# Kernel tuning notes

Measured on AMD Instinct MI355X. Metric: run time of the kernel, lower is better.

## Reference

```python
import jax, jax.numpy as jnp
import numpy as np

TEMPERATURE = 1.0  # init kwarg
B, D = 8192, 128


def setup_inputs() -> dict:
    key = jax.random.key(0)
    k1, k2 = jax.random.split(key)
    sk = jax.random.normal(k1, (B, D), dtype=jnp.float32)
    im = jax.random.normal(k2, (B, D), dtype=jnp.float32)
    return {"sk": sk, "im": im}


def reference(sk, im):
    # The torch module builds a [2B,2B] Euclidean distance matrix over the
    # interleaved [sk_0, im_0, sk_1, im_1, ...] rows, then via the eye-mask /
    # repeat_interleave / [:,1::2] / good_indices / [::2] gather chain selects,
    # for each anchor i, logits row = [-d(sk_i, im_i)/T] ++ [-d(sk_i, im_j)/T, j != i]
    # with label 0, followed by mean cross-entropy.  Since cross-entropy only
    # depends on {row values} and which entry is positive, this is exactly:
    #   loss = mean_i( logsumexp_j(-d(sk_i, im_j)/T) - (-d(sk_i, im_i)/T) )
    # so we only need the [B,B] sk-vs-im distance block (dist_type == 0).
    sq = (
        jnp.sum(sk * sk, axis=1)[:, None]
        + jnp.sum(im * im, axis=1)[None, :]
        - 2.0 * (sk @ im.T)
    )  # [B, B] squared distances
    d = jnp.sqrt(jnp.maximum(sq, 0.0))
    logits = -d / TEMPERATURE  # [B, B]
    lse = jax.nn.logsumexp(logits, axis=1)  # [B]
    loss = jnp.mean(lse - jnp.diagonal(logits))
    return loss
```

## Files before the change

kernel.cpp:

```cpp
#include <hip/hip_runtime.h>
#include <math.h>

#define NB 8192
#define ND 128
#define GSTEP 64
#define NSTEP 4
#define NJB 32

#define C2F 2.0813689810056077f
#define NC2 (-4.1627379620112154f)

typedef float f32x4 __attribute__((ext_vector_type(4)));

typedef __attribute__((address_space(3))) void lds_void_t;
typedef __attribute__((address_space(1))) const void gconst_void_t;

__device__ __forceinline__ unsigned f2bf(float f) {
    union { float f; unsigned u; } v; v.f = f;
    unsigned r = v.u + 0x7FFFu + ((v.u >> 16) & 1u);
    return r >> 16;
}

__global__ void __launch_bounds__(256) prep_kernel(
    const float* __restrict__ sk, const float* __restrict__ im,
    unsigned* __restrict__ skb8, unsigned* __restrict__ imb8,
    float* __restrict__ skn, float* __restrict__ imn,
    float* __restrict__ diag, float* __restrict__ gacc,
    unsigned* __restrict__ ticket) {
    if (blockIdx.x == 0 && threadIdx.x == 0) { *gacc = 0.f; *ticket = 0u; }
    const int wave = threadIdx.x >> 6, lane = threadIdx.x & 63;
    const int half = lane >> 5, l32 = lane & 31;
    const int row = blockIdx.x * 8 + wave * 2 + half;
    const size_t off = (size_t)row * 128 + l32 * 4;
    const float4 a = *reinterpret_cast<const float4*>(sk + off);
    const float4 b = *reinterpret_cast<const float4*>(im + off);
    unsigned pa = 0, pb = 0;
    pa = __builtin_amdgcn_cvt_pk_fp8_f32(a.x, a.y, pa, false);
    pa = __builtin_amdgcn_cvt_pk_fp8_f32(a.z, a.w, pa, true);
    pb = __builtin_amdgcn_cvt_pk_fp8_f32(b.x, b.y, pb, false);
    pb = __builtin_amdgcn_cvt_pk_fp8_f32(b.z, b.w, pb, true);
    skb8[row * 32 + l32] = pa;
    imb8[row * 32 + l32] = pb;
    float sa = a.x * a.x + a.y * a.y + a.z * a.z + a.w * a.w;
    float sb = b.x * b.x + b.y * b.y + b.z * b.z + b.w * b.w;
    float dx = a.x - b.x, dy = a.y - b.y, dz = a.z - b.z, dw = a.w - b.w;
    float sd = dx * dx + dy * dy + dz * dz + dw * dw;
#pragma unroll
    for (int st = 1; st < 32; st <<= 1) {
        sa += __shfl_xor(sa, st);
        sb += __shfl_xor(sb, st);
        sd += __shfl_xor(sd, st);
    }
    if (l32 == 0) {
        skn[row] = sa * C2F;
        imn[row] = sb * C2F;
        diag[row] = sqrtf(sd);
    }
}

__global__ void __launch_bounds__(256, 5) tile_kernel(
    const unsigned char* __restrict__ skb8, const unsigned char* __restrict__ imb8,
    const float* __restrict__ skn, const float* __restrict__ imn,
    float* __restrict__ partial) {
    __shared__ unsigned char Ast[2][GSTEP * ND];

    const int t = threadIdx.x;
    const int w = t >> 6, lane = t & 63;
    const int hi = lane >> 4, lo = lane & 15;
    const int iw = blockIdx.x * 128 + w * 32;
    const int jg0 = blockIdx.y * (GSTEP * NSTEP);

    long bfr[2][4];
#pragma unroll
    for (int n = 0; n < 2; ++n) {
        const unsigned char* bp = skb8 + (size_t)(iw + n * 16 + lo) * ND + hi * 8;
#pragma unroll
        for (int kk = 0; kk < 4; ++kk)
            bfr[n][kk] = *reinterpret_cast<const long*>(bp + kk * 32);
    }
    float skv[2];
#pragma unroll
    for (int n = 0; n < 2; ++n) skv[n] = skn[iw + n * 16 + lo];

#define STAGE_A(buf, jrow0)                                                       \
    {                                                                             \
        _Pragma("unroll")                                                         \
        for (int q = 0; q < 2; ++q) {                                             \
            const int rl = w * 16 + q * 8 + (lane >> 3);                          \
            const int sp = (lane & 7) ^ ((rl >> 1) & 7);                          \
            const unsigned char* gp = imb8 + (size_t)((jrow0) + rl) * ND + sp * 16;\
            __builtin_amdgcn_global_load_lds((gconst_void_t*)gp,                  \
                (lds_void_t*)(&Ast[(buf)][(w * 16 + q * 8) * ND]), 16, 0, 0);     \
        }                                                                         \
    }

    STAGE_A(0, jg0)
    __syncthreads();

    float sacc[2] = {0.f, 0.f};

    for (int s = 0; s < NSTEP; ++s) {
        const int jb = jg0 + s * GSTEP;
        if (s + 1 < NSTEP) STAGE_A((s + 1) & 1, jb + GSTEP)

        float imnv[4][4];
#pragma unroll
        for (int m = 0; m < 4; ++m) {
            float4 v = *reinterpret_cast<const float4*>(imn + jb + m * 16 + hi * 4);
            imnv[m][0] = v.x; imnv[m][1] = v.y; imnv[m][2] = v.z; imnv[m][3] = v.w;
        }

        f32x4 acc[4][2];
#pragma unroll
        for (int m = 0; m < 4; ++m)
#pragma unroll
            for (int n = 0; n < 2; ++n)
                acc[m][n] = (f32x4){0.f, 0.f, 0.f, 0.f};

        const char* Ab = (const char*)Ast[s & 1];
#pragma unroll
        for (int kk = 0; kk < 4; ++kk) {
            long af[4];
#pragma unroll
            for (int m = 0; m < 4; ++m)
                af[m] = *reinterpret_cast<const long*>(
                    Ab + (m * 16 + lo) * ND + (((kk * 4 + hi) ^ (lo & 14)) << 3));
#pragma unroll
            for (int m = 0; m < 4; ++m)
#pragma unroll
                for (int n = 0; n < 2; ++n)
                    acc[m][n] = __builtin_amdgcn_mfma_f32_16x16x32_fp8_fp8(
                        af[m], bfr[n][kk], acc[m][n], 0, 0, 0);
        }

#pragma unroll
        for (int n = 0; n < 2; ++n) {
            float ssum = 0.f;
#pragma unroll
            for (int m = 0; m < 4; ++m) {
#pragma unroll
                for (int r = 0; r < 4; ++r) {
                    float sq2 = fmaf(NC2, acc[m][n][r], skv[n]) + imnv[m][r];
                    float d2;
                    asm("v_sqrt_f32 %0, abs(%1)" : "=v"(d2) : "v"(sq2));
                    float e;
                    asm("v_exp_f32 %0, -%1" : "=v"(e) : "v"(d2));
                    ssum += e;
                }
            }
            sacc[n] += ssum;
        }
        __syncthreads();
    }

#pragma unroll
    for (int n = 0; n < 2; ++n) {
        sacc[n] += __shfl_xor(sacc[n], 16);
        sacc[n] += __shfl_xor(sacc[n], 32);
    }
    if (lane < 16) {
        partial[(size_t)blockIdx.y * NB + iw + lo] = sacc[0];
        partial[(size_t)blockIdx.y * NB + iw + 16 + lo] = sacc[1];
    }
#undef STAGE_A
}

__global__ void finalize_kernel(const float* __restrict__ partial,
                                const float* __restrict__ diag,
                                float* __restrict__ gacc, unsigned* __restrict__ ticket,
                                float* __restrict__ out) {
    const int i = blockIdx.x * 256 + threadIdx.x;
    float rs = 0.f;
#pragma unroll
    for (int c = 0; c < NJB; ++c) rs += partial[(size_t)c * NB + i];
    float v = __logf(rs) + diag[i];
    __shared__ float red[256];
    red[threadIdx.x] = v;
    __syncthreads();
    for (int st = 128; st > 0; st >>= 1) {
        if (threadIdx.x < st) red[threadIdx.x] += red[threadIdx.x + st];
        __syncthreads();
    }
    if (threadIdx.x == 0) {
        atomicAdd(gacc, red[0]);
        __threadfence();
        unsigned old = atomicAdd(ticket, 1u);
        if (old == (NB / 256) - 1) {
            float tot = atomicAdd(gacc, 0.f);
            out[0] = tot / (float)NB;
        }
    }
}

extern "C" void kernel_launch(void* const* d_in, const int* in_sizes, int n_in,
                              void* d_out, int out_size, void* d_ws, size_t ws_size,
                              hipStream_t stream) {
    const float* sk = (const float*)d_in[0];
    const float* im = (const float*)d_in[1];
    float* out = (float*)d_out;
    float* ws = (float*)d_ws;

    unsigned char* skb8 = (unsigned char*)ws;
    unsigned char* imb8 = skb8 + (size_t)NB * ND;
    float* fbase   = ws + (size_t)NB * ND / 2;
    float* skn     = fbase;
    float* imn     = fbase + NB;
    float* diag    = fbase + 2 * NB;
    float* partial = fbase + 3 * NB;
    float* gacc    = partial + (size_t)NJB * NB;
    unsigned* ticket = (unsigned*)(gacc + 1);

    prep_kernel<<<NB / 8, 256, 0, stream>>>(
        sk, im, (unsigned*)skb8, (unsigned*)imb8, skn, imn, diag, gacc, ticket);
    dim3 grid(NB / 128, NJB);
    tile_kernel<<<grid, 256, 0, stream>>>(skb8, imb8, skn, imn, partial);
    finalize_kernel<<<NB / 256, 256, 0, stream>>>(partial, diag, gacc, ticket, out);
}
```

Measured before the change: 89.17 us.

## Pre-swizzle fp8 operands into MFMA fragment layout and drop LDS staging

The prep kernel now writes the fp8 sk/im data directly in the per-lane MFMA fragment order, so each lane loads its 8-byte operand with one coalesced global load. The tile kernel drops LDS double-buffering and barriers and reads the A fragments straight from global/L2. The grid becomes 1D with each wave owning 32 rows and a group of 512 columns (NSTEP 8, NJB 16), and the occupancy hint drops to 4. This removes LDS traffic and barrier stalls but depends on L2 to serve the im data reused across waves, and without prefetching, load latency can become exposed.

```diff
diff --git a/kernel.cpp b/kernel.cpp
--- a/kernel.cpp
+++ b/kernel.cpp
@@ -4,104 +4,91 @@
 #define NB 8192
 #define ND 128
 #define GSTEP 64
-#define NSTEP 4
-#define NJB 32
+#define NSTEP 8
+#define NJB 16
 
 #define C2F 2.0813689810056077f
 #define NC2 (-4.1627379620112154f)
 
 typedef float f32x4 __attribute__((ext_vector_type(4)));
-
-typedef __attribute__((address_space(3))) void lds_void_t;
-typedef __attribute__((address_space(1))) const void gconst_void_t;
-
-__device__ __forceinline__ unsigned f2bf(float f) {
-    union { float f; unsigned u; } v; v.f = f;
-    unsigned r = v.u + 0x7FFFu + ((v.u >> 16) & 1u);
-    return r >> 16;
-}
+typedef unsigned long long ull;
 
 __global__ void __launch_bounds__(256) prep_kernel(
     const float* __restrict__ sk, const float* __restrict__ im,
-    unsigned* __restrict__ skb8, unsigned* __restrict__ imb8,
+    ull* __restrict__ skf, ull* __restrict__ imf,
     float* __restrict__ skn, float* __restrict__ imn,
     float* __restrict__ diag, float* __restrict__ gacc,
     unsigned* __restrict__ ticket) {
     if (blockIdx.x == 0 && threadIdx.x == 0) { *gacc = 0.f; *ticket = 0u; }
-    const int wave = threadIdx.x >> 6, lane = threadIdx.x & 63;
-    const int half = lane >> 5, l32 = lane & 31;
-    const int row = blockIdx.x * 8 + wave * 2 + half;
-    const size_t off = (size_t)row * 128 + l32 * 4;
-    const float4 a = *reinterpret_cast<const float4*>(sk + off);
-    const float4 b = *reinterpret_cast<const float4*>(im + off);
-    unsigned pa = 0, pb = 0;
-    pa = __builtin_amdgcn_cvt_pk_fp8_f32(a.x, a.y, pa, false);
-    pa = __builtin_amdgcn_cvt_pk_fp8_f32(a.z, a.w, pa, true);
-    pb = __builtin_amdgcn_cvt_pk_fp8_f32(b.x, b.y, pb, false);
-    pb = __builtin_amdgcn_cvt_pk_fp8_f32(b.z, b.w, pb, true);
-    skb8[row * 32 + l32] = pa;
-    imb8[row * 32 + l32] = pb;
-    float sa = a.x * a.x + a.y * a.y + a.z * a.z + a.w * a.w;
-    float sb = b.x * b.x + b.y * b.y + b.z * b.z + b.w * b.w;
-    float dx = a.x - b.x, dy = a.y - b.y, dz = a.z - b.z, dw = a.w - b.w;
-    float sd = dx * dx + dy * dy + dz * dz + dw * dw;
-#pragma unroll
-    for (int st = 1; st < 32; st <<= 1) {
+    const int gtid = blockIdx.x * 256 + threadIdx.x;
+    const int row = gtid >> 4;
+    const int j = gtid & 15;
+    const size_t off = (size_t)row * ND + j * 8;
+    const float4* a4 = reinterpret_cast<const float4*>(sk + off);
+    const float4* b4 = reinterpret_cast<const float4*>(im + off);
+    float4 a0 = a4[0], a1 = a4[1], b0 = b4[0], b1 = b4[1];
+
+    unsigned al = 0, ah = 0, bl = 0, bh = 0;
+    al = __builtin_amdgcn_cvt_pk_fp8_f32(a0.x, a0.y, al, false);
+    al = __builtin_amdgcn_cvt_pk_fp8_f32(a0.z, a0.w, al, true);
+    ah = __builtin_amdgcn_cvt_pk_fp8_f32(a1.x, a1.y, ah, false);
+    ah = __builtin_amdgcn_cvt_pk_fp8_f32(a1.z, a1.w, ah, true);
+    bl = __builtin_amdgcn_cvt_pk_fp8_f32(b0.x, b0.y, bl, false);
+    bl = __builtin_amdgcn_cvt_pk_fp8_f32(b0.z, b0.w, bl, true);
+    bh = __builtin_amdgcn_cvt_pk_fp8_f32(b1.x, b1.y, bh, false);
+    bh = __builtin_amdgcn_cvt_pk_fp8_f32(b1.z, b1.w, bh, true);
+
+    const size_t didx = (size_t)(row >> 4) * 256 + (j >> 2) * 64 + (j & 3) * 16 + (row & 15);
+    skf[didx] = (ull)al | ((ull)ah << 32);
+    imf[didx] = (ull)bl | ((ull)bh << 32);
+
+    float sa = a0.x*a0.x + a0.y*a0.y + a0.z*a0.z + a0.w*a0.w
+             + a1.x*a1.x + a1.y*a1.y + a1.z*a1.z + a1.w*a1.w;
+    float sb = b0.x*b0.x + b0.y*b0.y + b0.z*b0.z + b0.w*b0.w
+             + b1.x*b1.x + b1.y*b1.y + b1.z*b1.z + b1.w*b1.w;
+    float d0 = a0.x-b0.x, d1 = a0.y-b0.y, d2 = a0.z-b0.z, d3 = a0.w-b0.w;
+    float d4 = a1.x-b1.x, d5 = a1.y-b1.y, d6 = a1.z-b1.z, d7 = a1.w-b1.w;
+    float sd = d0*d0 + d1*d1 + d2*d2 + d3*d3 + d4*d4 + d5*d5 + d6*d6 + d7*d7;
+#pragma unroll
+    for (int st = 1; st < 16; st <<= 1) {
         sa += __shfl_xor(sa, st);
         sb += __shfl_xor(sb, st);
         sd += __shfl_xor(sd, st);
     }
-    if (l32 == 0) {
+    if (j == 0) {
         skn[row] = sa * C2F;
         imn[row] = sb * C2F;
         diag[row] = sqrtf(sd);
     }
 }
 
-__global__ void __launch_bounds__(256, 5) tile_kernel(
-    const unsigned char* __restrict__ skb8, const unsigned char* __restrict__ imb8,
+__global__ void __launch_bounds__(256, 4) tile_kernel(
+    const ull* __restrict__ skf, const ull* __restrict__ imf,
     const float* __restrict__ skn, const float* __restrict__ imn,
     float* __restrict__ partial) {
-    __shared__ unsigned char Ast[2][GSTEP * ND];
-
-    const int t = threadIdx.x;
-    const int w = t >> 6, lane = t & 63;
+    const int w = threadIdx.x >> 6, lane = threadIdx.x & 63;
     const int hi = lane >> 4, lo = lane & 15;
-    const int iw = blockIdx.x * 128 + w * 32;
-    const int jg0 = blockIdx.y * (GSTEP * NSTEP);
+    const int gw = blockIdx.x * 4 + w;
+    const int iw = (gw & 255) * 32;
+    const int jgrp = gw >> 8;
+    const int jg0 = jgrp * (GSTEP * NSTEP);
 
     long bfr[2][4];
-#pragma unroll
-    for (int n = 0; n < 2; ++n) {
-        const unsigned char* bp = skb8 + (size_t)(iw + n * 16 + lo) * ND + hi * 8;
+    const int gi = iw >> 4;
+#pragma unroll
+    for (int n = 0; n < 2; ++n)
 #pragma unroll
         for (int kk = 0; kk < 4; ++kk)
-            bfr[n][kk] = *reinterpret_cast<const long*>(bp + kk * 32);
-    }
+            bfr[n][kk] = (long)skf[(size_t)(gi + n) * 256 + kk * 64 + lane];
     float skv[2];
 #pragma unroll
     for (int n = 0; n < 2; ++n) skv[n] = skn[iw + n * 16 + lo];
-
-#define STAGE_A(buf, jrow0)                                                       \
-    {                                                                             \
-        _Pragma("unroll")                                                         \
-        for (int q = 0; q < 2; ++q) {                                             \
-            const int rl = w * 16 + q * 8 + (lane >> 3);                          \
-            const int sp = (lane & 7) ^ ((rl >> 1) & 7);                          \
-            const unsigned char* gp = imb8 + (size_t)((jrow0) + rl) * ND + sp * 16;\
-            __builtin_amdgcn_global_load_lds((gconst_void_t*)gp,                  \
-                (lds_void_t*)(&Ast[(buf)][(w * 16 + q * 8) * ND]), 16, 0, 0);     \
-        }                                                                         \
-    }
-
-    STAGE_A(0, jg0)
-    __syncthreads();
 
     float sacc[2] = {0.f, 0.f};
 
     for (int s = 0; s < NSTEP; ++s) {
         const int jb = jg0 + s * GSTEP;
-        if (s + 1 < NSTEP) STAGE_A((s + 1) & 1, jb + GSTEP)
+        const size_t ga = (size_t)(jb >> 4) * 256;
 
         float imnv[4][4];
 #pragma unroll
@@ -117,14 +104,12 @@
             for (int n = 0; n < 2; ++n)
                 acc[m][n] = (f32x4){0.f, 0.f, 0.f, 0.f};
 
-        const char* Ab = (const char*)Ast[s & 1];
 #pragma unroll
         for (int kk = 0; kk < 4; ++kk) {
             long af[4];
 #pragma unroll
             for (int m = 0; m < 4; ++m)
-                af[m] = *reinterpret_cast<const long*>(
-                    Ab + (m * 16 + lo) * ND + (((kk * 4 + hi) ^ (lo & 14)) << 3));
+                af[m] = (long)imf[ga + (size_t)m * 256 + kk * 64 + lane];
 #pragma unroll
             for (int m = 0; m < 4; ++m)
 #pragma unroll
@@ -150,7 +135,6 @@
             }
             sacc[n] += ssum;
         }
-        __syncthreads();
     }
 
 #pragma unroll
@@ -159,10 +143,9 @@
         sacc[n] += __shfl_xor(sacc[n], 32);
     }
     if (lane < 16) {
-        partial[(size_t)blockIdx.y * NB + iw + lo] = sacc[0];
-        partial[(size_t)blockIdx.y * NB + iw + 16 + lo] = sacc[1];
-    }
-#undef STAGE_A
+        partial[(size_t)jgrp * NB + iw + lo] = sacc[0];
+        partial[(size_t)jgrp * NB + iw + 16 + lo] = sacc[1];
+    }
 }
 
 __global__ void finalize_kernel(const float* __restrict__ partial,
@@ -200,8 +183,8 @@
     float* out = (float*)d_out;
     float* ws = (float*)d_ws;
 
-    unsigned char* skb8 = (unsigned char*)ws;
-    unsigned char* imb8 = skb8 + (size_t)NB * ND;
+    ull* skf = (ull*)ws;
+    ull* imf = skf + (size_t)NB * ND / 8;
     float* fbase   = ws + (size_t)NB * ND / 2;
     float* skn     = fbase;
     float* imn     = fbase + NB;
@@ -210,9 +193,8 @@
     float* gacc    = partial + (size_t)NJB * NB;
     unsigned* ticket = (unsigned*)(gacc + 1);
 
-    prep_kernel<<<NB / 8, 256, 0, stream>>>(
-        sk, im, (unsigned*)skb8, (unsigned*)imb8, skn, imn, diag, gacc, ticket);
-    dim3 grid(NB / 128, NJB);
-    tile_kernel<<<grid, 256, 0, stream>>>(skb8, imb8, skn, imn, partial);
+    prep_kernel<<<NB * 16 / 256, 256, 0, stream>>>(
+        sk, im, skf, imf, skn, imn, diag, gacc, ticket);
+    tile_kernel<<<1024, 256, 0, stream>>>(skf, imf, skn, imn, partial);
     finalize_kernel<<<NB / 256, 256, 0, stream>>>(partial, diag, gacc, ticket, out);
 }
```

Result: no change. 87.51 us (-1.9%).
